# Performance work log

Hardware: AMD Instinct MI355X
Metric: run time of the kernel (lower is better)

Reference implementation:

```python
import jax, jax.numpy as jnp
import numpy as np

N = 100000
E = 800000
D_IN = 128
D_OUT = 128
EPS = 1e-5


def setup_inputs() -> dict:
    key = jax.random.key(0)
    k = jax.random.split(key, 7)
    x = jax.random.normal(k[0], (N, D_IN), dtype=jnp.float32)
    edge_index = jax.random.randint(k[1], (2, E), 0, N, dtype=jnp.int64)
    # kaiming_uniform(a=sqrt(5)) on [out,in] -> bound = 1/sqrt(in_dim)
    bound = 1.0 / np.sqrt(D_IN)
    W_self = jax.random.uniform(k[2], (D_OUT, D_IN), minval=-bound, maxval=bound, dtype=jnp.float32)
    W_neigh = jax.random.uniform(k[3], (D_OUT, D_IN), minval=-bound, maxval=bound, dtype=jnp.float32)
    bias = jnp.zeros((D_OUT,), dtype=jnp.float32)
    gamma = jnp.ones((D_OUT,), dtype=jnp.float32)
    beta = jnp.zeros((D_OUT,), dtype=jnp.float32)
    return {"x": x, "edge_index": edge_index, "W_self": W_self,
            "W_neigh": W_neigh, "bias": bias, "gamma": gamma, "beta": beta}


def reference(x, edge_index, W_self, W_neigh, bias, gamma, beta):
    src, dst = edge_index[0], edge_index[1]
    # mean neighbor aggregation: segment-sum of gathered features / clamped degree
    agg = jax.ops.segment_sum(x[src], dst, num_segments=N)          # [N, D_IN]
    deg = jax.ops.segment_sum(jnp.ones_like(dst, dtype=x.dtype), dst, num_segments=N)
    neigh_mean = agg / jnp.maximum(deg, 1.0)[:, None]
    # dual linear + bias + ReLU
    out = jnp.einsum('nd,od->no', x, W_self) + jnp.einsum('nd,od->no', neigh_mean, W_neigh) + bias
    h = jax.nn.relu(out)
    # LayerNorm over last dim
    mu = jnp.mean(h, axis=-1, keepdims=True)
    var = jnp.var(h, axis=-1, keepdims=True)
    return (h - mu) * jax.lax.rsqrt(var + EPS) * gamma + beta
```

## Files before the change

### kernel.cpp

```cpp
#include <hip/hip_runtime.h>
#include <hip/hip_bf16.h>

#define N_NODES 100000
#define E_EDGES 800000
#define LN_EPS 1e-5f
#define WPAD 264

#define P_BLOCKS 256
#define EPB 3125
#define SLICE 64
#define NBK 1563
#define NBK_PAD 1792
#define OFFS_STRIDE 1564
#define QCAP 768
#define CONV_PER_BLOCK 12500

typedef __attribute__((ext_vector_type(4))) float f32x4;
typedef __attribute__((ext_vector_type(8))) short short8;

__device__ __forceinline__ unsigned short f2bf(float f) {
    __hip_bfloat16 h = __float2bfloat16(f);
    return *reinterpret_cast<unsigned short*>(&h);
}
__device__ __forceinline__ float bflo(unsigned int u) { return __uint_as_float(u << 16); }
__device__ __forceinline__ float bfhi(unsigned int u) { return __uint_as_float(u & 0xffff0000u); }

__global__ __launch_bounds__(256) void fill_part1(
    const float* __restrict__ x, const int* __restrict__ ei,
    unsigned short* __restrict__ xb, unsigned int* __restrict__ gstore,
    unsigned short* __restrict__ offs)
{
    const int t = threadIdx.x, b = blockIdx.x;
    if (b >= P_BLOCKS) {
        const float4* x4 = reinterpret_cast<const float4*>(x);
        ushort4* xb4 = reinterpret_cast<ushort4*>(xb);
        const int j0 = (b - P_BLOCKS) * CONV_PER_BLOCK;
        for (int j = t; j < CONV_PER_BLOCK; j += 256) {
            float4 v = x4[j0 + j];
            ushort4 o;
            o.x = f2bf(v.x); o.y = f2bf(v.y); o.z = f2bf(v.z); o.w = f2bf(v.w);
            xb4[j0 + j] = o;
        }
        return;
    }
    __shared__ unsigned long long eds[EPB];
    __shared__ unsigned int sorted_l[EPB];
    __shared__ int hist[NBK_PAD];
    __shared__ int starts[NBK_PAD + 1];
    __shared__ int partial[256];
    for (int i = t; i < NBK_PAD; i += 256) hist[i] = 0;
    __syncthreads();
    const int e0 = b * EPB;
    for (int i = t; i < EPB; i += 256) {
        unsigned src = (unsigned)ei[e0 + i];
        unsigned dst = (unsigned)ei[E_EDGES + e0 + i];
        unsigned bk = dst >> 6;
        eds[i] = ((unsigned long long)bk << 32) | (src << 6) | (dst & 63u);
        atomicAdd(&hist[bk], 1);
    }
    __syncthreads();
    int h[7], s = 0;
#pragma unroll
    for (int k = 0; k < 7; ++k) { h[k] = hist[t * 7 + k]; s += h[k]; }
    partial[t] = s;
    __syncthreads();
    for (int off = 1; off < 256; off <<= 1) {
        int v = (t >= off) ? partial[t - off] : 0;
        __syncthreads();
        partial[t] += v;
        __syncthreads();
    }
    int run = partial[t] - s;
#pragma unroll
    for (int k = 0; k < 7; ++k) { starts[t * 7 + k] = run; run += h[k]; }
    if (t == 255) starts[NBK_PAD] = run;
    __syncthreads();
    for (int i = t; i < NBK_PAD; i += 256) hist[i] = 0;
    __syncthreads();
    for (int i = t; i < EPB; i += 256) {
        unsigned long long u = eds[i];
        unsigned bk = (unsigned)(u >> 32);
        int p = starts[bk] + atomicAdd(&hist[bk], 1);
        sorted_l[p] = (unsigned int)u;
    }
    __syncthreads();
    for (int i = t; i < EPB; i += 256)
        gstore[b * EPB + i] = sorted_l[i];
    for (int i = t; i < OFFS_STRIDE; i += 256)
        offs[b * OFFS_STRIDE + i] = (unsigned short)starts[i];
}

__global__ __launch_bounds__(256) void agg2(
    const unsigned int* __restrict__ gstore, const unsigned short* __restrict__ offs,
    const unsigned short* __restrict__ xb, unsigned short* __restrict__ nb)
{
    __shared__ unsigned int sortedq[QCAP];
    __shared__ int cnt_l[SLICE];
    __shared__ int run_l[SLICE];
    __shared__ int qs_l[SLICE + 1];
    const int t = threadIdx.x, b = blockIdx.x;
    if (t < SLICE) { cnt_l[t] = 0; run_l[t] = 0; }
    __syncthreads();
    const int s0 = offs[t * OFFS_STRIDE + b];
    const int s1 = offs[t * OFFS_STRIDE + b + 1];
    const unsigned int* myrun = gstore + t * EPB;
    for (int j = s0; j < s1; ++j)
        atomicAdd(&cnt_l[myrun[j] & 63u], 1);
    __syncthreads();
    if (t < SLICE) {
        int inc = cnt_l[t];
        for (int off = 1; off < 64; off <<= 1) {
            int u = __shfl_up(inc, off);
            if (t >= off) inc += u;
        }
        qs_l[t + 1] = inc;
        if (t == 0) qs_l[0] = 0;
    }
    __syncthreads();
    for (int j = s0; j < s1; ++j) {
        unsigned rec = myrun[j];
        int p = qs_l[rec & 63u] + atomicAdd(&run_l[rec & 63u], 1);
        if (p < QCAP) sortedq[p] = rec;
    }
    __syncthreads();
    const int wave = t >> 6, lane = t & 63;
    const int subi = lane >> 4, chunk = lane & 15;
    const uint4* x4 = reinterpret_cast<const uint4*>(xb);
    for (int ln = wave * 16; ln < wave * 16 + 16; ++ln) {
        const int qb = qs_l[ln], cc = qs_l[ln + 1] - qb;
        float acc[8];
#pragma unroll
        for (int k = 0; k < 8; ++k) acc[k] = 0.f;
        for (int i = 0; i < cc; i += 4) {
            int idx = i + subi;
            if (idx < cc) {
                unsigned rec = sortedq[qb + idx];
                uint4 v = x4[(rec >> 6) * 16 + chunk];
                acc[0] += bflo(v.x); acc[1] += bfhi(v.x);
                acc[2] += bflo(v.y); acc[3] += bfhi(v.y);
                acc[4] += bflo(v.z); acc[5] += bfhi(v.z);
                acc[6] += bflo(v.w); acc[7] += bfhi(v.w);
            }
        }
#pragma unroll
        for (int k = 0; k < 8; ++k) {
            acc[k] += __shfl_xor(acc[k], 16);
            acc[k] += __shfl_xor(acc[k], 32);
        }
        const int node = b * SLICE + ln;
        if (subi == 0 && node < N_NODES) {
            float inv = 1.0f / (float)(cc > 1 ? cc : 1);
            uint4 o;
            o.x = ((unsigned)f2bf(acc[1] * inv) << 16) | f2bf(acc[0] * inv);
            o.y = ((unsigned)f2bf(acc[3] * inv) << 16) | f2bf(acc[2] * inv);
            o.z = ((unsigned)f2bf(acc[5] * inv) << 16) | f2bf(acc[4] * inv);
            o.w = ((unsigned)f2bf(acc[7] * inv) << 16) | f2bf(acc[6] * inv);
            reinterpret_cast<uint4*>(nb)[node * 16 + chunk] = o;
        }
    }
}

__global__ __launch_bounds__(256, 2) void fused_mfma(
    const unsigned short* __restrict__ xb, const unsigned short* __restrict__ nb,
    const float* __restrict__ Wself, const float* __restrict__ Wneigh,
    const float* __restrict__ bias, const float* __restrict__ gamma,
    const float* __restrict__ beta, float* __restrict__ out)
{
    __shared__ unsigned short WT[128][WPAD];
    const int t = threadIdx.x;
    const float4* Ws4 = reinterpret_cast<const float4*>(Wself);
    const float4* Wn4 = reinterpret_cast<const float4*>(Wneigh);
    for (int idx = t; idx < 4096; idx += 256) {
        int n = idx >> 5, k4 = (idx & 31) << 2;
        float4 a = Ws4[idx];
        float4 b = Wn4[idx];
        ushort4 ua, ub;
        ua.x = f2bf(a.x); ua.y = f2bf(a.y); ua.z = f2bf(a.z); ua.w = f2bf(a.w);
        ub.x = f2bf(b.x); ub.y = f2bf(b.y); ub.z = f2bf(b.z); ub.w = f2bf(b.w);
        *reinterpret_cast<ushort4*>(&WT[n][k4]) = ua;
        *reinterpret_cast<ushort4*>(&WT[n][128 + k4]) = ub;
    }
    __syncthreads();

    const int lane = t & 63, wave = t >> 6;
    const int l16 = lane & 15, quad = lane >> 4;
    float bia[8], gam[8], bet[8];
#pragma unroll
    for (int n = 0; n < 8; ++n) {
        int col = n * 16 + l16;
        bia[n] = bias[col]; gam[n] = gamma[col]; bet[n] = beta[col];
    }

    const int ntiles = (N_NODES + 255) / 256;
    for (int tile = blockIdx.x; tile < ntiles; tile += gridDim.x) {
        const int rowbase = tile * 256 + wave * 64;
        f32x4 acc[4][8];
#pragma unroll
        for (int m = 0; m < 4; ++m)
#pragma unroll
            for (int n = 0; n < 8; ++n) acc[m][n] = (f32x4)0.f;
        int rows[4];
#pragma unroll
        for (int m = 0; m < 4; ++m) {
            int r = rowbase + m * 16 + l16;
            rows[m] = r < N_NODES ? r : N_NODES - 1;
        }
#pragma unroll
        for (int kstep = 0; kstep < 8; ++kstep) {
            const unsigned short* Asrc = (kstep < 4) ? xb : nb;
            const int koff = (kstep & 3) * 32 + quad * 8;
            short8 a[4];
#pragma unroll
            for (int m = 0; m < 4; ++m)
                a[m] = *reinterpret_cast<const short8*>(Asrc + rows[m] * 128 + koff);
#pragma unroll
            for (int n = 0; n < 8; ++n) {
                short8 b = *reinterpret_cast<const short8*>(&WT[n * 16 + l16][kstep * 32 + quad * 8]);
#pragma unroll
                for (int m = 0; m < 4; ++m)
                    acc[m][n] = __builtin_amdgcn_mfma_f32_16x16x32_bf16(a[m], b, acc[m][n], 0, 0, 0);
            }
        }
#pragma unroll
        for (int m = 0; m < 4; ++m) {
#pragma unroll
            for (int r = 0; r < 4; ++r) {
                float h[8], s = 0.f, q = 0.f;
#pragma unroll
                for (int n = 0; n < 8; ++n) {
                    float v = acc[m][n][r] + bia[n];
                    v = fmaxf(v, 0.f);
                    h[n] = v; s += v; q += v * v;
                }
#pragma unroll
                for (int msk = 1; msk <= 8; msk <<= 1) {
                    s += __shfl_xor(s, msk);
                    q += __shfl_xor(q, msk);
                }
                const float mu = s * (1.f / 128.f);
                const float var = q * (1.f / 128.f) - mu * mu;
                const float rs = rsqrtf(var + LN_EPS);
                const int R = rowbase + m * 16 + quad * 4 + r;
                if (R < N_NODES) {
#pragma unroll
                    for (int n = 0; n < 8; ++n)
                        out[R * 128 + n * 16 + l16] = (h[n] - mu) * rs * gam[n] + bet[n];
                }
            }
        }
    }
}

extern "C" void kernel_launch(void* const* d_in, const int* in_sizes, int n_in,
                              void* d_out, int out_size, void* d_ws, size_t ws_size,
                              hipStream_t stream) {
    const float* x      = (const float*)d_in[0];
    const int*   ei     = (const int*)d_in[1];
    const float* Wself  = (const float*)d_in[2];
    const float* Wneigh = (const float*)d_in[3];
    const float* bias   = (const float*)d_in[4];
    const float* gamma  = (const float*)d_in[5];
    const float* beta   = (const float*)d_in[6];
    float* out = (float*)d_out;

    char* ws = (char*)d_ws;
    unsigned short* xb = (unsigned short*)ws;
    unsigned short* nb = (unsigned short*)(ws + 25600000);
    unsigned int* gstore = (unsigned int*)(ws + 51200000);
    unsigned short* offs = (unsigned short*)(ws + 54400000);

    fill_part1<<<512, 256, 0, stream>>>(x, ei, xb, gstore, offs);
    agg2<<<NBK, 256, 0, stream>>>(gstore, offs, xb, nb);
    const int ntiles = (N_NODES + 255) / 256;
    fused_mfma<<<ntiles, 256, 0, stream>>>(xb, nb, Wself, Wneigh, bias, gamma, beta, out);
}
```

Measured before the change: 204.8 us.

## Restructure edge bucketing, staged aggregation and small-tile MFMA with global bf16 weights

The partition kernel now runs 512 threads per block. It counts histograms straight from the edge array, replaces the barrier-heavy prefix scan with a wave-shuffle scan, and packs start and end offsets into one 32-bit word. It also converts the weights to bf16 once into a global buffer. The aggregation kernel does a cooperative prefix over the per-partition run lengths, stages the records into LDS, and then counts and scatters from LDS in parallel instead of each thread looping serially. The MFMA kernel drops its per-block LDS weight transpose and uses 64-row blocks over 1563 blocks, loading B fragments from global or L2. This trades the old A-fragment reuse across four m tiles for more parallelism and no LDS setup.

```diff
diff --git a/kernel.cpp b/kernel.cpp
--- a/kernel.cpp
+++ b/kernel.cpp
@@ -4,16 +4,15 @@
 #define N_NODES 100000
 #define E_EDGES 800000
 #define LN_EPS 1e-5f
-#define WPAD 264
 
 #define P_BLOCKS 256
 #define EPB 3125
 #define SLICE 64
 #define NBK 1563
-#define NBK_PAD 1792
-#define OFFS_STRIDE 1564
+#define NBK_PAD 2048
 #define QCAP 768
-#define CONV_PER_BLOCK 12500
+#define CONV_BLOCKS 128
+#define CONV_PER_BLOCK 25000
 
 typedef __attribute__((ext_vector_type(4))) float f32x4;
 typedef __attribute__((ext_vector_type(8))) short short8;
@@ -25,105 +24,135 @@
 __device__ __forceinline__ float bflo(unsigned int u) { return __uint_as_float(u << 16); }
 __device__ __forceinline__ float bfhi(unsigned int u) { return __uint_as_float(u & 0xffff0000u); }
 
-__global__ __launch_bounds__(256) void fill_part1(
-    const float* __restrict__ x, const int* __restrict__ ei,
+__global__ __launch_bounds__(512) void part1(
+    const float* __restrict__ x, const float* __restrict__ Ws,
+    const float* __restrict__ Wn, const int* __restrict__ ei,
     unsigned short* __restrict__ xb, unsigned int* __restrict__ gstore,
-    unsigned short* __restrict__ offs)
+    unsigned int* __restrict__ offs32, unsigned short* __restrict__ Bt)
 {
     const int t = threadIdx.x, b = blockIdx.x;
     if (b >= P_BLOCKS) {
+        const int cb = b - P_BLOCKS;
         const float4* x4 = reinterpret_cast<const float4*>(x);
         ushort4* xb4 = reinterpret_cast<ushort4*>(xb);
-        const int j0 = (b - P_BLOCKS) * CONV_PER_BLOCK;
-        for (int j = t; j < CONV_PER_BLOCK; j += 256) {
+        const int j0 = cb * CONV_PER_BLOCK;
+        for (int j = t; j < CONV_PER_BLOCK; j += 512) {
             float4 v = x4[j0 + j];
             ushort4 o;
             o.x = f2bf(v.x); o.y = f2bf(v.y); o.z = f2bf(v.z); o.w = f2bf(v.w);
             xb4[j0 + j] = o;
         }
+        if (cb == 0) {
+            const float4* Ws4 = reinterpret_cast<const float4*>(Ws);
+            const float4* Wn4 = reinterpret_cast<const float4*>(Wn);
+            ushort4* Bt4 = reinterpret_cast<ushort4*>(Bt);
+            for (int idx = t; idx < 8192; idx += 512) {
+                int n = idx >> 6, g = idx & 63;
+                float4 v = (g < 32) ? Ws4[n * 32 + g] : Wn4[n * 32 + (g - 32)];
+                ushort4 o;
+                o.x = f2bf(v.x); o.y = f2bf(v.y); o.z = f2bf(v.z); o.w = f2bf(v.w);
+                Bt4[idx] = o;
+            }
+        }
         return;
     }
-    __shared__ unsigned long long eds[EPB];
     __shared__ unsigned int sorted_l[EPB];
     __shared__ int hist[NBK_PAD];
-    __shared__ int starts[NBK_PAD + 1];
-    __shared__ int partial[256];
-    for (int i = t; i < NBK_PAD; i += 256) hist[i] = 0;
-    __syncthreads();
+    __shared__ int wsum[8];
+    const int lane = t & 63, wid = t >> 6;
     const int e0 = b * EPB;
-    for (int i = t; i < EPB; i += 256) {
+    for (int i = t; i < NBK_PAD; i += 512) hist[i] = 0;
+    __syncthreads();
+    for (int i = t; i < EPB; i += 512)
+        atomicAdd(&hist[((unsigned)ei[E_EDGES + e0 + i]) >> 6], 1);
+    __syncthreads();
+    int h[4], s = 0;
+#pragma unroll
+    for (int k = 0; k < 4; ++k) { h[k] = hist[t * 4 + k]; s += h[k]; }
+    int inc = s;
+#pragma unroll
+    for (int off = 1; off < 64; off <<= 1) {
+        int u = __shfl_up(inc, off);
+        if (lane >= off) inc += u;
+    }
+    if (lane == 63) wsum[wid] = inc;
+    __syncthreads();
+    int wbase = 0;
+#pragma unroll
+    for (int w = 0; w < 8; ++w) if (w < wid) wbase += wsum[w];
+    unsigned st[5];
+    st[0] = wbase + inc - s;
+#pragma unroll
+    for (int k = 0; k < 4; ++k) st[k + 1] = st[k] + h[k];
+#pragma unroll
+    for (int k = 0; k < 4; ++k) {
+        int idx = t * 4 + k;
+        if (idx < NBK) offs32[b * NBK + idx] = st[k] | (st[k + 1] << 16);
+        hist[idx] = (int)st[k];
+    }
+    __syncthreads();
+    for (int i = t; i < EPB; i += 512) {
         unsigned src = (unsigned)ei[e0 + i];
         unsigned dst = (unsigned)ei[E_EDGES + e0 + i];
-        unsigned bk = dst >> 6;
-        eds[i] = ((unsigned long long)bk << 32) | (src << 6) | (dst & 63u);
-        atomicAdd(&hist[bk], 1);
-    }
-    __syncthreads();
-    int h[7], s = 0;
-#pragma unroll
-    for (int k = 0; k < 7; ++k) { h[k] = hist[t * 7 + k]; s += h[k]; }
-    partial[t] = s;
-    __syncthreads();
-    for (int off = 1; off < 256; off <<= 1) {
-        int v = (t >= off) ? partial[t - off] : 0;
-        __syncthreads();
-        partial[t] += v;
-        __syncthreads();
-    }
-    int run = partial[t] - s;
-#pragma unroll
-    for (int k = 0; k < 7; ++k) { starts[t * 7 + k] = run; run += h[k]; }
-    if (t == 255) starts[NBK_PAD] = run;
-    __syncthreads();
-    for (int i = t; i < NBK_PAD; i += 256) hist[i] = 0;
-    __syncthreads();
-    for (int i = t; i < EPB; i += 256) {
-        unsigned long long u = eds[i];
-        unsigned bk = (unsigned)(u >> 32);
-        int p = starts[bk] + atomicAdd(&hist[bk], 1);
-        sorted_l[p] = (unsigned int)u;
-    }
-    __syncthreads();
-    for (int i = t; i < EPB; i += 256)
+        int p = atomicAdd(&hist[dst >> 6], 1);
+        sorted_l[p] = (src << 6) | (dst & 63u);
+    }
+    __syncthreads();
+    for (int i = t; i < EPB; i += 512)
         gstore[b * EPB + i] = sorted_l[i];
-    for (int i = t; i < OFFS_STRIDE; i += 256)
-        offs[b * OFFS_STRIDE + i] = (unsigned short)starts[i];
 }
 
 __global__ __launch_bounds__(256) void agg2(
-    const unsigned int* __restrict__ gstore, const unsigned short* __restrict__ offs,
+    const unsigned int* __restrict__ gstore, const unsigned int* __restrict__ offs32,
     const unsigned short* __restrict__ xb, unsigned short* __restrict__ nb)
 {
+    __shared__ unsigned int stage[QCAP];
     __shared__ unsigned int sortedq[QCAP];
-    __shared__ int cnt_l[SLICE];
-    __shared__ int run_l[SLICE];
-    __shared__ int qs_l[SLICE + 1];
+    __shared__ int cnt_l[SLICE], run_l[SLICE], qs_l[SLICE + 1];
+    __shared__ int wsum[4];
     const int t = threadIdx.x, b = blockIdx.x;
+    const int lane = t & 63, wid = t >> 6;
     if (t < SLICE) { cnt_l[t] = 0; run_l[t] = 0; }
-    __syncthreads();
-    const int s0 = offs[t * OFFS_STRIDE + b];
-    const int s1 = offs[t * OFFS_STRIDE + b + 1];
-    const unsigned int* myrun = gstore + t * EPB;
-    for (int j = s0; j < s1; ++j)
-        atomicAdd(&cnt_l[myrun[j] & 63u], 1);
+    const unsigned int v = offs32[t * NBK + b];
+    const int s0 = (int)(v & 0xffffu), len = (int)(v >> 16) - s0;
+    int inc = len;
+#pragma unroll
+    for (int off = 1; off < 64; off <<= 1) {
+        int u = __shfl_up(inc, off);
+        if (lane >= off) inc += u;
+    }
+    if (lane == 63) wsum[wid] = inc;
+    __syncthreads();
+    int wbase = 0;
+#pragma unroll
+    for (int w = 0; w < 4; ++w) if (w < wid) wbase += wsum[w];
+    int pos = wbase + inc - len;
+    int total = wsum[0] + wsum[1] + wsum[2] + wsum[3];
+    if (total > QCAP) total = QCAP;
+    const unsigned int* myrun = gstore + t * EPB + s0;
+    for (int k = 0; k < len; ++k)
+        if (pos + k < QCAP) stage[pos + k] = myrun[k];
+    __syncthreads();
+    for (int i = t; i < total; i += 256)
+        atomicAdd(&cnt_l[stage[i] & 63u], 1);
     __syncthreads();
     if (t < SLICE) {
-        int inc = cnt_l[t];
+        int ic = cnt_l[t];
         for (int off = 1; off < 64; off <<= 1) {
-            int u = __shfl_up(inc, off);
-            if (t >= off) inc += u;
-        }
-        qs_l[t + 1] = inc;
+            int u = __shfl_up(ic, off);
+            if (t >= off) ic += u;
+        }
+        qs_l[t + 1] = ic;
         if (t == 0) qs_l[0] = 0;
     }
     __syncthreads();
-    for (int j = s0; j < s1; ++j) {
-        unsigned rec = myrun[j];
+    for (int i = t; i < total; i += 256) {
+        unsigned rec = stage[i];
         int p = qs_l[rec & 63u] + atomicAdd(&run_l[rec & 63u], 1);
-        if (p < QCAP) sortedq[p] = rec;
-    }
-    __syncthreads();
-    const int wave = t >> 6, lane = t & 63;
+        sortedq[p] = rec;
+    }
+    __syncthreads();
+    const int wave = t >> 6;
     const int subi = lane >> 4, chunk = lane & 15;
     const uint4* x4 = reinterpret_cast<const uint4*>(xb);
     for (int ln = wave * 16; ln < wave * 16 + 16; ++ln) {
@@ -135,11 +164,11 @@
             int idx = i + subi;
             if (idx < cc) {
                 unsigned rec = sortedq[qb + idx];
-                uint4 v = x4[(rec >> 6) * 16 + chunk];
-                acc[0] += bflo(v.x); acc[1] += bfhi(v.x);
-                acc[2] += bflo(v.y); acc[3] += bfhi(v.y);
-                acc[4] += bflo(v.z); acc[5] += bfhi(v.z);
-                acc[6] += bflo(v.w); acc[7] += bfhi(v.w);
+                uint4 vv = x4[(rec >> 6) * 16 + chunk];
+                acc[0] += bflo(vv.x); acc[1] += bfhi(vv.x);
+                acc[2] += bflo(vv.y); acc[3] += bfhi(vv.y);
+                acc[4] += bflo(vv.z); acc[5] += bfhi(vv.z);
+                acc[6] += bflo(vv.w); acc[7] += bfhi(vv.w);
             }
         }
 #pragma unroll
@@ -160,93 +189,61 @@
     }
 }
 
-__global__ __launch_bounds__(256, 2) void fused_mfma(
+__global__ __launch_bounds__(256) void fused2(
     const unsigned short* __restrict__ xb, const unsigned short* __restrict__ nb,
-    const float* __restrict__ Wself, const float* __restrict__ Wneigh,
+    const unsigned short* __restrict__ Bt,
     const float* __restrict__ bias, const float* __restrict__ gamma,
     const float* __restrict__ beta, float* __restrict__ out)
 {
-    __shared__ unsigned short WT[128][WPAD];
     const int t = threadIdx.x;
-    const float4* Ws4 = reinterpret_cast<const float4*>(Wself);
-    const float4* Wn4 = reinterpret_cast<const float4*>(Wneigh);
-    for (int idx = t; idx < 4096; idx += 256) {
-        int n = idx >> 5, k4 = (idx & 31) << 2;
-        float4 a = Ws4[idx];
-        float4 b = Wn4[idx];
-        ushort4 ua, ub;
-        ua.x = f2bf(a.x); ua.y = f2bf(a.y); ua.z = f2bf(a.z); ua.w = f2bf(a.w);
-        ub.x = f2bf(b.x); ub.y = f2bf(b.y); ub.z = f2bf(b.z); ub.w = f2bf(b.w);
-        *reinterpret_cast<ushort4*>(&WT[n][k4]) = ua;
-        *reinterpret_cast<ushort4*>(&WT[n][128 + k4]) = ub;
-    }
-    __syncthreads();
-
     const int lane = t & 63, wave = t >> 6;
     const int l16 = lane & 15, quad = lane >> 4;
+    const int base = blockIdx.x * 64 + wave * 16;
+    int row = base + l16;
+    if (row >= N_NODES) row = N_NODES - 1;
     float bia[8], gam[8], bet[8];
 #pragma unroll
     for (int n = 0; n < 8; ++n) {
         int col = n * 16 + l16;
         bia[n] = bias[col]; gam[n] = gamma[col]; bet[n] = beta[col];
     }
-
-    const int ntiles = (N_NODES + 255) / 256;
-    for (int tile = blockIdx.x; tile < ntiles; tile += gridDim.x) {
-        const int rowbase = tile * 256 + wave * 64;
-        f32x4 acc[4][8];
-#pragma unroll
-        for (int m = 0; m < 4; ++m)
-#pragma unroll
-            for (int n = 0; n < 8; ++n) acc[m][n] = (f32x4)0.f;
-        int rows[4];
-#pragma unroll
-        for (int m = 0; m < 4; ++m) {
-            int r = rowbase + m * 16 + l16;
-            rows[m] = r < N_NODES ? r : N_NODES - 1;
-        }
-#pragma unroll
-        for (int kstep = 0; kstep < 8; ++kstep) {
-            const unsigned short* Asrc = (kstep < 4) ? xb : nb;
-            const int koff = (kstep & 3) * 32 + quad * 8;
-            short8 a[4];
-#pragma unroll
-            for (int m = 0; m < 4; ++m)
-                a[m] = *reinterpret_cast<const short8*>(Asrc + rows[m] * 128 + koff);
-#pragma unroll
-            for (int n = 0; n < 8; ++n) {
-                short8 b = *reinterpret_cast<const short8*>(&WT[n * 16 + l16][kstep * 32 + quad * 8]);
-#pragma unroll
-                for (int m = 0; m < 4; ++m)
-                    acc[m][n] = __builtin_amdgcn_mfma_f32_16x16x32_bf16(a[m], b, acc[m][n], 0, 0, 0);
-            }
-        }
-#pragma unroll
-        for (int m = 0; m < 4; ++m) {
-#pragma unroll
-            for (int r = 0; r < 4; ++r) {
-                float h[8], s = 0.f, q = 0.f;
-#pragma unroll
-                for (int n = 0; n < 8; ++n) {
-                    float v = acc[m][n][r] + bia[n];
-                    v = fmaxf(v, 0.f);
-                    h[n] = v; s += v; q += v * v;
-                }
-#pragma unroll
-                for (int msk = 1; msk <= 8; msk <<= 1) {
-                    s += __shfl_xor(s, msk);
-                    q += __shfl_xor(q, msk);
-                }
-                const float mu = s * (1.f / 128.f);
-                const float var = q * (1.f / 128.f) - mu * mu;
-                const float rs = rsqrtf(var + LN_EPS);
-                const int R = rowbase + m * 16 + quad * 4 + r;
-                if (R < N_NODES) {
-#pragma unroll
-                    for (int n = 0; n < 8; ++n)
-                        out[R * 128 + n * 16 + l16] = (h[n] - mu) * rs * gam[n] + bet[n];
-                }
-            }
+    f32x4 acc[8];
+#pragma unroll
+    for (int n = 0; n < 8; ++n) acc[n] = (f32x4)0.f;
+#pragma unroll
+    for (int kstep = 0; kstep < 8; ++kstep) {
+        const unsigned short* Asrc = (kstep < 4) ? xb : nb;
+        const int koff = (kstep & 3) * 32 + quad * 8;
+        short8 a = *reinterpret_cast<const short8*>(Asrc + row * 128 + koff);
+#pragma unroll
+        for (int n = 0; n < 8; ++n) {
+            short8 bb = *reinterpret_cast<const short8*>(
+                Bt + (n * 16 + l16) * 256 + kstep * 32 + quad * 8);
+            acc[n] = __builtin_amdgcn_mfma_f32_16x16x32_bf16(a, bb, acc[n], 0, 0, 0);
+        }
+    }
+#pragma unroll
+    for (int r = 0; r < 4; ++r) {
+        float h[8], s = 0.f, q = 0.f;
+#pragma unroll
+        for (int n = 0; n < 8; ++n) {
+            float v = acc[n][r] + bia[n];
+            v = fmaxf(v, 0.f);
+            h[n] = v; s += v; q += v * v;
+        }
+#pragma unroll
+        for (int msk = 1; msk <= 8; msk <<= 1) {
+            s += __shfl_xor(s, msk);
+            q += __shfl_xor(q, msk);
+        }
+        const float mu = s * (1.f / 128.f);
+        const float var = q * (1.f / 128.f) - mu * mu;
+        const float rs = rsqrtf(var + LN_EPS);
+        const int R = base + quad * 4 + r;
+        if (R < N_NODES) {
+#pragma unroll
+            for (int n = 0; n < 8; ++n)
+                out[R * 128 + n * 16 + l16] = (h[n] - mu) * rs * gam[n] + bet[n];
         }
     }
 }
@@ -267,10 +264,11 @@
     unsigned short* xb = (unsigned short*)ws;
     unsigned short* nb = (unsigned short*)(ws + 25600000);
     unsigned int* gstore = (unsigned int*)(ws + 51200000);
-    unsigned short* offs = (unsigned short*)(ws + 54400000);
-
-    fill_part1<<<512, 256, 0, stream>>>(x, ei, xb, gstore, offs);
-    agg2<<<NBK, 256, 0, stream>>>(gstore, offs, xb, nb);
-    const int ntiles = (N_NODES + 255) / 256;
-    fused_mfma<<<ntiles, 256, 0, stream>>>(xb, nb, Wself, Wneigh, bias, gamma, beta, out);
-}
+    unsigned int* offs32 = (unsigned int*)(ws + 54400000);
+    unsigned short* Bt = (unsigned short*)(ws + 56000512);
+
+    part1<<<P_BLOCKS + CONV_BLOCKS, 512, 0, stream>>>(x, Wself, Wneigh, ei,
+                                                      xb, gstore, offs32, Bt);
+    agg2<<<NBK, 256, 0, stream>>>(gstore, offs32, xb, nb);
+    fused2<<<NBK, 256, 0, stream>>>(xb, nb, Bt, bias, gamma, beta, out);
+}
```

Result: slower. 241.1 us (+17.8%).
